# Kernel tuning notes

Hardware: AMD Instinct MI355X
Metric: run time of the kernel (lower is better)

## Reference

```python
import jax, jax.numpy as jnp
import numpy as np
import math

B, L, DIM, H = 2, 2048, 512, 8


def setup_inputs() -> dict:
    key = jax.random.key(0)
    ks = jax.random.split(key, 8)
    s = 0.02
    return {
        "x": jax.random.normal(ks[0], (B, L, DIM), dtype=jnp.float32),
        "Wq": jax.random.normal(ks[1], (DIM, DIM), dtype=jnp.float32) * s,
        "Wk": jax.random.normal(ks[2], (DIM, DIM), dtype=jnp.float32) * s,
        "Wv": jax.random.normal(ks[3], (DIM, DIM), dtype=jnp.float32) * s,
        "Wb": jax.random.normal(ks[4], (H, DIM), dtype=jnp.float32) * s,   # content_bias weight
        "mixing": jax.random.normal(ks[5], (H, DIM), dtype=jnp.float32) * 0.2,  # UNIFORM init, std=0.2
        "Wd": jax.random.normal(ks[6], (DIM, DIM), dtype=jnp.float32) * s,
        "bd": jax.random.normal(ks[7], (DIM,), dtype=jnp.float32) * s,
    }


def reference(x, Wq, Wk, Wv, Wb, mixing, Wd, bd):
    b, l, d = x.shape
    h = mixing.shape[0]
    dh = d // h
    q = x @ Wq.T                      # [B,L,D]
    k = x @ Wk.T                      # [B,S,D]
    v = (x @ Wv.T).reshape(b, l, h, dh).transpose(0, 2, 1, 3)  # [B,H,S,dh]
    # scores[b,h,l,s] = sum_d q[b,l,d] * mixing[h,d] * k[b,s,d]
    scores = jnp.einsum("bld,hd,bsd->bhls", q, mixing, k)
    # content bias: [B,S,H] -> broadcast over query positions as [B,H,1,S]
    cb = jnp.einsum("bsd,hd->bhs", x, Wb)
    scale = math.sqrt(d / h)  # attention_head_size = dim / num_heads
    scores = (scores + cb[:, :, None, :]) / scale
    probs = jax.nn.softmax(scores, axis=-1)   # dropout disabled (eval)
    ctx = jnp.einsum("bhls,bhsd->bhld", probs, v)  # [B,H,L,dh]
    ctx = ctx.transpose(0, 2, 1, 3).reshape(b, l, d)
    return ctx @ Wd.T + bd
```

## Files before the change

kernel.cpp:

```cpp
#include <hip/hip_runtime.h>

#define B_ 2
#define L_ 2048
#define D_ 512
#define H_ 8
#define S_ 2048

typedef __attribute__((ext_vector_type(8))) short short8;
typedef __attribute__((ext_vector_type(8))) unsigned short ushort8;
typedef __attribute__((ext_vector_type(4))) unsigned short ushort4v;
typedef __attribute__((ext_vector_type(4))) float f32x4;
typedef __attribute__((ext_vector_type(16))) float f32x16;
typedef __attribute__((ext_vector_type(4))) float float4v;
typedef __attribute__((ext_vector_type(8))) _Float16 half8;
typedef __attribute__((ext_vector_type(4))) _Float16 half4;

__device__ __forceinline__ unsigned short f2bf(float f) {
    unsigned u = __float_as_uint(f);
    u += 0x7FFF + ((u >> 16) & 1);
    return (unsigned short)(u >> 16);
}
__device__ __forceinline__ float bf2f(unsigned short s) {
    return __uint_as_float(((unsigned)s) << 16);
}
__device__ __forceinline__ unsigned char f2fp8(float f) {
    return (unsigned char)(__builtin_amdgcn_cvt_pk_fp8_f32(f, f, 0, false) & 0xff);
}
__device__ __forceinline__ long pack8fp8(const float* v) {
    int lo = __builtin_amdgcn_cvt_pk_fp8_f32(v[0], v[1], 0, false);
    lo = __builtin_amdgcn_cvt_pk_fp8_f32(v[2], v[3], lo, true);
    int hi = __builtin_amdgcn_cvt_pk_fp8_f32(v[4], v[5], 0, false);
    hi = __builtin_amdgcn_cvt_pk_fp8_f32(v[6], v[7], hi, true);
    union { int i[2]; long l; } u;
    u.i[0] = lo; u.i[1] = hi;
    return u.l;
}
__device__ __forceinline__ int swap23(int x) {
    return (x & ~12) | ((x & 4) << 1) | ((x & 8) >> 1);
}
__device__ __forceinline__ void async16(void* lds, const void* g) {
    __builtin_amdgcn_global_load_lds(
        (const __attribute__((address_space(1))) void*)(g),
        (__attribute__((address_space(3))) void*)(lds), 16, 0, 0);
}

__global__ __launch_bounds__(256) void cvt_cb(const float* __restrict__ x,
                                              const float* __restrict__ w0, const float* __restrict__ w1,
                                              const float* __restrict__ w2, const float* __restrict__ w3,
                                              const float* __restrict__ Wb,
                                              unsigned short* __restrict__ xb,
                                              unsigned short* __restrict__ d0, unsigned short* __restrict__ d1,
                                              unsigned short* __restrict__ d2, unsigned short* __restrict__ d3,
                                              float* __restrict__ cbf) {
    if (blockIdx.x < 3072) {
        int i = blockIdx.x * 256 + threadIdx.x;
        const float* s;
        unsigned short* d;
        int idx;
        if (i < 524288) { s = x; d = xb; idx = i; }
        else {
            int off = i - 524288;
            int wsel = off >> 16; idx = off & 65535;
            s = (wsel == 0) ? w0 : (wsel == 1) ? w1 : (wsel == 2) ? w2 : w3;
            d = (wsel == 0) ? d0 : (wsel == 1) ? d1 : (wsel == 2) ? d2 : d3;
        }
        float4v v = *(const float4v*)(s + (size_t)idx * 4);
        ushort4v o;
        o[0] = f2bf(v[0]); o[1] = f2bf(v[1]); o[2] = f2bf(v[2]); o[3] = f2bf(v[3]);
        *(ushort4v*)(d + (size_t)idx * 4) = o;
    } else {
        const int tid = threadIdx.x, w = tid >> 6, lane = tid & 63;
        const int row = (blockIdx.x - 3072) * 4 + w;
        const int h = lane >> 3, seg = lane & 7;
        const float* xp = x + (size_t)row * 512 + seg * 64;
        const float* wp = Wb + (size_t)h * 512 + seg * 64;
        float acc = 0.f;
        #pragma unroll
        for (int j = 0; j < 16; ++j) {
            float4v xv = *(const float4v*)(xp + j * 4);
            float4v wv = *(const float4v*)(wp + j * 4);
            acc += xv[0] * wv[0] + xv[1] * wv[1] + xv[2] * wv[2] + xv[3] * wv[3];
        }
        acc += __shfl_xor(acc, 1);
        acc += __shfl_xor(acc, 2);
        acc += __shfl_xor(acc, 4);
        if (seg == 0) {
            int b = row >> 11, s = row & 2047;
            int T = s >> 5, off = s & 31;
            int r2 = off & 3, k = off >> 2;
            int u = (k & 1) + ((k >> 2) << 1), hi2 = (k >> 1) & 1;
            int R = 4 * u + r2;
            cbf[((size_t)((b * 8 + h) * 64 + T)) * 32 + hi2 * 16 + R] = acc * 0.125f * 1.44269504f;
        }
    }
}

__device__ __forceinline__ void gemm128_core(const unsigned short* __restrict__ Ap,
                                             const unsigned short* __restrict__ Bp,
                                             short* sA, short* sB, int tid, f32x4 c[4][4]) {
    const int w = tid >> 6, lane = tid & 63, quad = lane >> 4, l15 = lane & 15;
    const int wm = (w >> 1) * 64, wn = (w & 1) * 64;
    for (int kc = 0; kc < 8; ++kc) {
        __syncthreads();
        #pragma unroll
        for (int j = 0; j < 4; ++j) {
            int i = tid + j * 256;
            int row = i >> 3, seg = i & 7;
            *(ushort8*)&sA[row * 72 + seg * 8] = *(const ushort8*)(Ap + (size_t)row * 512 + kc * 64 + seg * 8);
            *(ushort8*)&sB[row * 72 + seg * 8] = *(const ushort8*)(Bp + (size_t)row * 512 + kc * 64 + seg * 8);
        }
        __syncthreads();
        #pragma unroll
        for (int ks = 0; ks < 2; ++ks) {
            short8 a[4], b[4];
            #pragma unroll
            for (int ii = 0; ii < 4; ++ii)
                a[ii] = *(const short8*)&sA[(wm + ii * 16 + l15) * 72 + ks * 32 + quad * 8];
            #pragma unroll
            for (int jj = 0; jj < 4; ++jj)
                b[jj] = *(const short8*)&sB[(wn + jj * 16 + l15) * 72 + ks * 32 + quad * 8];
            #pragma unroll
            for (int ii = 0; ii < 4; ++ii)
                #pragma unroll
                for (int jj = 0; jj < 4; ++jj)
                    c[ii][jj] = __builtin_amdgcn_mfma_f32_16x16x32_bf16(a[ii], b[jj], c[ii][jj], 0, 0, 0);
        }
    }
}

__global__ __launch_bounds__(256) void gemm_qkv(const unsigned short* __restrict__ xb,
                                                const unsigned short* __restrict__ Wqb,
                                                const unsigned short* __restrict__ Wkb,
                                                const unsigned short* __restrict__ Wvb,
                                                unsigned short* __restrict__ qb,
                                                unsigned char* __restrict__ kpack8,
                                                unsigned short* __restrict__ vfrag) {
    __shared__ char sAB[2][32768];
    const int m0 = blockIdx.x * 128, n0 = blockIdx.y * 128, z = blockIdx.z;
    const unsigned short* Bsel = (z == 0) ? Wqb : ((z == 1) ? Wkb : Wvb);
    const int tid = threadIdx.x, w = tid >> 6, lane = tid & 63, quad = lane >> 4, l15 = lane & 15;
    const int wm = (w >> 1) * 64, wn = (w & 1) * 64;
    const char* Ab = (const char*)(xb + (size_t)m0 * 512);
    const char* Bb = (const char*)(Bsel + (size_t)n0 * 512);
    const int srow = tid >> 3;
    const int csw = (tid & 7) ^ (srow & 7);
    const size_t srcOff = (size_t)srow * 1024 + (size_t)csw * 16;
    auto stage = [&](int kc, int bi) {
        char* ba = &sAB[bi][0];
        #pragma unroll
        for (int j = 0; j < 4; ++j)
            async16(ba + j * 4096 + w * 1024, Ab + (size_t)j * 32768 + kc * 128 + srcOff);
        #pragma unroll
        for (int j = 0; j < 4; ++j)
            async16(ba + 16384 + j * 4096 + w * 1024, Bb + (size_t)j * 32768 + kc * 128 + srcOff);
    };

    f32x4 c[4][4];
    #pragma unroll
    for (int ii = 0; ii < 4; ++ii)
        #pragma unroll
        for (int jj = 0; jj < 4; ++jj) { f32x4 zv = {0.f, 0.f, 0.f, 0.f}; c[ii][jj] = zv; }

    stage(0, 0);
    for (int kc = 0; kc < 8; ++kc) {
        __syncthreads();
        if (kc < 7) stage(kc + 1, (kc + 1) & 1);
        const char* tA = &sAB[kc & 1][0];
        const char* tB = &sAB[kc & 1][16384];
        #pragma unroll
        for (int ks = 0; ks < 2; ++ks) {
            short8 a[4], b[4];
            #pragma unroll
            for (int ii = 0; ii < 4; ++ii) {
                int row = wm + ii * 16 + l15;
                a[ii] = *(const short8*)(tA + row * 128 + (((ks * 4 + quad) ^ (l15 & 7)) * 16));
            }
            #pragma unroll
            for (int jj = 0; jj < 4; ++jj) {
                int row = wn + jj * 16 + l15;
                b[jj] = *(const short8*)(tB + row * 128 + (((ks * 4 + quad) ^ (l15 & 7)) * 16));
            }
            #pragma unroll
            for (int ii = 0; ii < 4; ++ii)
                #pragma unroll
                for (int jj = 0; jj < 4; ++jj)
                    c[ii][jj] = __builtin_amdgcn_mfma_f32_16x16x32_bf16(a[ii], b[jj], c[ii][jj], 0, 0, 0);
        }
    }

    #pragma unroll
    for (int ii = 0; ii < 4; ++ii) {
        const int mb = m0 + wm + ii * 16 + quad * 4;
        const int bb = mb >> 11;
        if (z == 0) {
            #pragma unroll
            for (int jj = 0; jj < 4; ++jj) {
                int ncol = n0 + wn + jj * 16 + l15;
                #pragma unroll
                for (int r = 0; r < 4; ++r)
                    qb[(size_t)(mb + r) * 512 + ncol] = f2bf(c[ii][jj][r]);
            }
        } else if (z == 1) {
            #pragma unroll
            for (int jj = 0; jj < 4; ++jj) {
                int d = n0 + wn + jj * 16 + l15;
                int pair = d >> 5, fh = (d >> 4) & 1, hid = (d >> 3) & 1, jq = d & 7;
                #pragma unroll
                for (int r = 0; r < 4; ++r) {
                    int s = (mb + r) & 2047;
                    int t = s >> 5, rr = swap23(s & 31);
                    kpack8[(((size_t)(bb * 64 + t) * 16 + pair) << 10)
                           + (hid * 32 + rr) * 16 + fh * 8 + jq] = f2fp8(c[ii][jj][r] * 32.f);
                }
            }
        } else {
            const int hh = (n0 + wn) >> 6;
            const int s = mb & 2047;
            #pragma unroll
            for (int jj = 0; jj < 4; ++jj) {
                int dh = jj * 16 + l15;
                ushort4v o;
                o[0] = f2bf(c[ii][jj][0]); o[1] = f2bf(c[ii][jj][1]);
                o[2] = f2bf(c[ii][jj][2]); o[3] = f2bf(c[ii][jj][3]);
                size_t blk = ((size_t)(bb * H_ + hh) * 64 + (s >> 5)) * 4
                           + ((dh >> 5) * 2 + ((s >> 4) & 1));
                *(ushort4v*)(vfrag + blk * 512 + (dh & 31) * 8 + ((s >> 3) & 1) * 256 + (s & 7)) = o;
            }
        }
    }
}

__global__ __launch_bounds__(256) void gemm_out(const _Float16* __restrict__ Opart,
                                                const float* __restrict__ lpart,
                                                const unsigned short* __restrict__ Wdb,
                                                const float* __restrict__ bd,
                                                float* __restrict__ out) {
    __shared__ short sA[128 * 72];
    __shared__ short sB[128 * 72];
    const int m0 = blockIdx.x * 128, n0 = blockIdx.y * 128;
    const int tid = threadIdx.x, w = tid >> 6, lane = tid & 63, quad = lane >> 4, l15 = lane & 15;
    const int wm = (w >> 1) * 64, wn = (w & 1) * 64;
    f32x4 c[4][4];
    #pragma unroll
    for (int ii = 0; ii < 4; ++ii)
        #pragma unroll
        for (int jj = 0; jj < 4; ++jj) { f32x4 zv = {0.f, 0.f, 0.f, 0.f}; c[ii][jj] = zv; }
    for (int kc = 0; kc < 8; ++kc) {
        __syncthreads();
        #pragma unroll
        for (int j = 0; j < 4; ++j) {
            int i = tid + j * 256;
            int row = i >> 3, seg = i & 7;
            int gq = m0 + row;
            int b = gq >> 11, ql = gq & 2047, qq = ql & 127;
            int base = ((ql >> 7) << 5) | (kc << 2) | (b << 1);
            const _Float16* o0 = Opart + ((size_t)base << 13) + qq * 64 + seg * 8;
            float l = lpart[(size_t)base * 128 + qq] + lpart[(size_t)(base + 1) * 128 + qq];
            float inv = __builtin_amdgcn_rcpf(l);
            half8 v0 = *(const half8*)o0;
            half8 v1 = *(const half8*)(o0 + 8192);
            ushort8 ov;
            #pragma unroll
            for (int e = 0; e < 8; ++e)
                ov[e] = f2bf(((float)v0[e] + (float)v1[e]) * inv);
            *(ushort8*)&sA[row * 72 + seg * 8] = ov;
            *(ushort8*)&sB[row * 72 + seg * 8] =
                *(const ushort8*)(Wdb + (size_t)(n0 + row) * 512 + kc * 64 + seg * 8);
        }
        __syncthreads();
        #pragma unroll
        for (int ks = 0; ks < 2; ++ks) {
            short8 a[4], b2[4];
            #pragma unroll
            for (int ii = 0; ii < 4; ++ii)
                a[ii] = *(const short8*)&sA[(wm + ii * 16 + l15) * 72 + ks * 32 + quad * 8];
            #pragma unroll
            for (int jj = 0; jj < 4; ++jj)
                b2[jj] = *(const short8*)&sB[(wn + jj * 16 + l15) * 72 + ks * 32 + quad * 8];
            #pragma unroll
            for (int ii = 0; ii < 4; ++ii)
                #pragma unroll
                for (int jj = 0; jj < 4; ++jj)
                    c[ii][jj] = __builtin_amdgcn_mfma_f32_16x16x32_bf16(a[ii], b2[jj], c[ii][jj], 0, 0, 0);
        }
    }
    #pragma unroll
    for (int ii = 0; ii < 4; ++ii) {
        const int mb = m0 + wm + ii * 16 + quad * 4;
        #pragma unroll
        for (int jj = 0; jj < 4; ++jj) {
            int ncol = n0 + wn + jj * 16 + l15;
            float bias = bd[ncol];
            #pragma unroll
            for (int r = 0; r < 4; ++r)
                out[(size_t)(mb + r) * 512 + ncol] = c[ii][jj][r] + bias;
        }
    }
}

__global__ __launch_bounds__(256, 2) void flash_attn(const unsigned short* __restrict__ qb,
                                                     const unsigned char* __restrict__ kpack8,
                                                     const unsigned short* __restrict__ vfrag,
                                                     const float* __restrict__ cbf_all,
                                                     const float* __restrict__ mixing,
                                                     _Float16* __restrict__ Opart,
                                                     float* __restrict__ lpart) {
    __shared__ char sK[3][16384];
    const int bid = blockIdx.x;
    const int half = bid & 1, b = (bid >> 1) & 1, h = (bid >> 2) & 7, qt = bid >> 5;
    const int tid = threadIdx.x, w = tid >> 6, lane = tid & 63;
    const int l31 = lane & 31, hi = lane >> 5;
    const int q0 = qt * 128 + w * 32;
    const unsigned short* vfb = vfrag + ((size_t)(b * H_ + h) * 64 + half * 32) * 2048;
    const float* cbfb = cbf_all + ((size_t)((b * 8 + h) * 64 + half * 32)) * 32 + hi * 16;
    const float* mixh = mixing + h * D_;
    const float SC = 1.44269504f / 4096.0f;

    long qq[32];
    {
        const unsigned short* qrow = qb + ((size_t)(b * L_) + q0 + l31) * D_ + hi * 8;
        #pragma unroll
        for (int i = 0; i < 32; ++i) {
            ushort8 qv = *(const ushort8*)(qrow + i * 16);
            float4v ma = *(const float4v*)(mixh + i * 16 + hi * 8);
            float4v mb = *(const float4v*)(mixh + i * 16 + hi * 8 + 4);
            float v[8];
            v[0] = bf2f(qv[0]) * ma[0] * 16.f;
            v[1] = bf2f(qv[1]) * ma[1] * 16.f;
            v[2] = bf2f(qv[2]) * ma[2] * 16.f;
            v[3] = bf2f(qv[3]) * ma[3] * 16.f;
            v[4] = bf2f(qv[4]) * mb[0] * 16.f;
            v[5] = bf2f(qv[5]) * mb[1] * 16.f;
            v[6] = bf2f(qv[6]) * mb[2] * 16.f;
            v[7] = bf2f(qv[7]) * mb[3] * 16.f;
            qq[i] = pack8fp8(v);
        }
    }
    asm volatile("s_waitcnt vmcnt(0)" ::: "memory");

    f32x16 acco0, acco1;
    #pragma unroll
    for (int i = 0; i < 16; ++i) { acco0[i] = 0.f; acco1[i] = 0.f; }
    float lsum = 0.f;
    f32x16 aA0, aB0, aA1, aB1;
    short8 av00, av01, av10, av11;
    float4v cbf0, cbf1, cbf2, cbf3;

    auto stageK2 = [&](int t, int bi) {
        const char* src = (const char*)kpack8 + (((size_t)(b * 64 + half * 32 + t)) << 14);
        char* dst = &sK[bi][0];
        #pragma unroll
        for (int ii = 0; ii < 4; ++ii)
            async16(dst + w * 1024 + ii * 4096, src + w * 1024 + ii * 4096 + (size_t)lane * 16);
    };
    auto ldV = [&](int t) {
        const unsigned short* vp = vfb + (size_t)t * 2048 + lane * 8;
        av00 = *(const short8*)(vp);
        av01 = *(const short8*)(vp + 512);
        av10 = *(const short8*)(vp + 1024);
        av11 = *(const short8*)(vp + 1536);
        asm volatile("" ::: "memory");
    };
    auto ldCB = [&](int t) {
        const float* cp = cbfb + t * 32;
        cbf0 = *(const float4v*)(cp);
        cbf1 = *(const float4v*)(cp + 4);
        cbf2 = *(const float4v*)(cp + 8);
        cbf3 = *(const float4v*)(cp + 12);
        asm volatile("" ::: "memory");
    };
    auto cbfv = [&](int R) -> float {
        return (R < 4) ? cbf0[R & 3] : (R < 8) ? cbf1[R & 3] : (R < 12) ? cbf2[R & 3] : cbf3[R & 3];
    };
    auto pack_pv = [&](const float* pex) {
        union { unsigned int u[4]; short8 s8; } P0, P1;
        #pragma unroll
        for (int j = 0; j < 4; ++j) {
            P0.u[j] = __builtin_amdgcn_perm(__float_as_uint(pex[2 * j + 1]) + 0x8000u,
                                            __float_as_uint(pex[2 * j]) + 0x8000u, 0x07060302u);
            P1.u[j] = __builtin_amdgcn_perm(__float_as_uint(pex[8 + 2 * j + 1]) + 0x8000u,
                                            __float_as_uint(pex[8 + 2 * j]) + 0x8000u, 0x07060302u);
        }
        acco0 = __builtin_amdgcn_mfma_f32_32x32x16_bf16(av00, P0.s8, acco0, 0, 0, 0);
        acco0 = __builtin_amdgcn_mfma_f32_32x32x16_bf16(av01, P1.s8, acco0, 0, 0, 0);
        acco1 = __builtin_amdgcn_mfma_f32_32x32x16_bf16(av10, P0.s8, acco1, 0, 0, 0);
        acco1 = __builtin_amdgcn_mfma_f32_32x32x16_bf16(av11, P1.s8, acco1, 0, 0, 0);
    };
    auto tile_fused = [&](const char* buf, int T, f32x16& CA, f32x16& CB,
                          const f32x16& PA, const f32x16& PB) {
        __builtin_amdgcn_s_setprio(1);
        float pex[16];
        float lsA = 0.f, lsB = 0.f;
        #pragma unroll
        for (int fp = 0; fp < 16; ++fp) {
            const long* ap = (const long*)&buf[fp * 1024 + lane * 16];
            long a0 = ap[0], a1 = ap[1];
            CA = __builtin_amdgcn_mfma_f32_32x32x16_fp8_fp8(a0, qq[2 * fp], CA, 0, 0, 0);
            CB = __builtin_amdgcn_mfma_f32_32x32x16_fp8_fp8(a1, qq[2 * fp + 1], CB, 0, 0, 0);
            if (fp < 8) {
                float x0 = fmaf(PA[2 * fp] + PB[2 * fp], SC, cbfv(2 * fp));
                float x1 = fmaf(PA[2 * fp + 1] + PB[2 * fp + 1], SC, cbfv(2 * fp + 1));
                float e0, e1;
                asm("v_exp_f32 %0, %1" : "=v"(e0) : "v"(x0));
                asm("v_exp_f32 %0, %1" : "=v"(e1) : "v"(x1));
                pex[2 * fp] = e0; pex[2 * fp + 1] = e1;
                lsA += e0; lsB += e1;
            }
            if (fp == 8) { lsum += lsA + lsB; pack_pv(pex); }
            if (fp == 9)  ldV(T);
            if (fp == 10) ldCB(T);
        }
        __builtin_amdgcn_s_setprio(0);
    };
    auto tile_plain = [&](const char* buf, int T, f32x16& CA, f32x16& CB) {
        __builtin_amdgcn_s_setprio(1);
        #pragma unroll
        for (int fp = 0; fp < 16; ++fp) {
            const long* ap = (const long*)&buf[fp * 1024 + lane * 16];
            long a0 = ap[0], a1 = ap[1];
            CA = __builtin_amdgcn_mfma_f32_32x32x16_fp8_fp8(a0, qq[2 * fp], CA, 0, 0, 0);
            CB = __builtin_amdgcn_mfma_f32_32x32x16_fp8_fp8(a1, qq[2 * fp + 1], CB, 0, 0, 0);
            if (fp == 9)  ldV(T);
            if (fp == 10) ldCB(T);
        }
        __builtin_amdgcn_s_setprio(0);
    };
    auto sm_pv = [&](const f32x16& PA, const f32x16& PB) {
        float pex[16];
        float lsA = 0.f, lsB = 0.f;
        #pragma unroll
        for (int R = 0; R < 16; R += 2) {
            float x0 = fmaf(PA[R] + PB[R], SC, cbfv(R));
            float x1 = fmaf(PA[R + 1] + PB[R + 1], SC, cbfv(R + 1));
            float e0, e1;
            asm("v_exp_f32 %0, %1" : "=v"(e0) : "v"(x0));
            asm("v_exp_f32 %0, %1" : "=v"(e1) : "v"(x1));
            pex[R] = e0; pex[R + 1] = e1;
            lsA += e0; lsB += e1;
        }
        lsum += lsA + lsB;
        pack_pv(pex);
    };
    auto zero16 = [](f32x16& v) {
        #pragma unroll
        for (int i = 0; i < 16; ++i) v[i] = 0.f;
    };

    stageK2(0, 0); stageK2(1, 1);

    zero16(aA0); zero16(aB0);
    asm volatile("s_waitcnt vmcnt(4)" ::: "memory");
    __builtin_amdgcn_s_barrier();
    tile_plain(&sK[0][0], 0, aA0, aB0);
    stageK2(2, 2);

    int cur = 1;
    for (int t = 1; t <= 30; t += 2) {
        zero16(aA1); zero16(aB1);
        asm volatile("s_waitcnt vmcnt(4)" ::: "memory");
        __builtin_amdgcn_s_barrier();
        tile_fused(&sK[cur][0], t, aA1, aB1, aA0, aB0);
        if (t + 2 <= 31) stageK2(t + 2, (cur + 2 >= 3) ? cur - 1 : cur + 2);
        cur = (cur == 2) ? 0 : cur + 1;

        zero16(aA0); zero16(aB0);
        asm volatile("s_waitcnt vmcnt(4)" ::: "memory");
        __builtin_amdgcn_s_barrier();
        tile_fused(&sK[cur][0], t + 1, aA0, aB0, aA1, aB1);
        if (t + 3 <= 31) stageK2(t + 3, (cur + 2 >= 3) ? cur - 1 : cur + 2);
        cur = (cur == 2) ? 0 : cur + 1;
    }

    {
        zero16(aA1); zero16(aB1);
        asm volatile("s_waitcnt vmcnt(0)" ::: "memory");
        __builtin_amdgcn_s_barrier();
        tile_fused(&sK[cur][0], 31, aA1, aB1, aA0, aB0);
        asm volatile("s_waitcnt vmcnt(0)" ::: "memory");
        sm_pv(aA1, aB1);
    }

    lsum += __shfl_xor(lsum, 32);
    if (hi == 0) lpart[(size_t)bid * 128 + w * 32 + l31] = lsum;
    {
        _Float16* sO = (_Float16*)&sK[0][0];
        const int q = w * 32 + l31;
        #pragma unroll
        for (int u = 0; u < 4; ++u) {
            half4 v0, v1;
            v0[0] = (_Float16)acco0[4 * u];     v0[1] = (_Float16)acco0[4 * u + 1];
            v0[2] = (_Float16)acco0[4 * u + 2]; v0[3] = (_Float16)acco0[4 * u + 3];
            v1[0] = (_Float16)acco1[4 * u];     v1[1] = (_Float16)acco1[4 * u + 1];
            v1[2] = (_Float16)acco1[4 * u + 2]; v1[3] = (_Float16)acco1[4 * u + 3];
            *(half4*)&sO[q * 72 + u * 8 + 4 * hi]      = v0;
            *(half4*)&sO[q * 72 + 32 + u * 8 + 4 * hi] = v1;
        }
        const int qd = tid >> 1, hf = tid & 1;
        _Float16* dst = Opart + ((size_t)bid << 13) + qd * 64 + hf * 32;
        const _Float16* srcp = sO + qd * 72 + hf * 32;
        #pragma unroll
        for (int k = 0; k < 4; ++k)
            *(half8*)(dst + k * 8) = *(const half8*)(srcp + k * 8);
    }
}

extern "C" void kernel_launch(void* const* d_in, const int* in_sizes, int n_in,
                              void* d_out, int out_size, void* d_ws, size_t ws_size,
                              hipStream_t stream) {
    (void)in_sizes; (void)n_in; (void)out_size; (void)ws_size;
    const float* x      = (const float*)d_in[0];
    const float* Wq     = (const float*)d_in[1];
    const float* Wk     = (const float*)d_in[2];
    const float* Wv     = (const float*)d_in[3];
    const float* Wb     = (const float*)d_in[4];
    const float* mixing = (const float*)d_in[5];
    const float* Wd     = (const float*)d_in[6];
    const float* bd     = (const float*)d_in[7];
    float* out = (float*)d_out;

    char* ws = (char*)d_ws;
    const size_t MiB = 1048576;
    unsigned short* xb     = (unsigned short*)(ws);
    unsigned short* qb     = (unsigned short*)(ws + 4 * MiB);
    unsigned char*  kpack8 = (unsigned char*)(ws + 8 * MiB);
    unsigned short* vfrag  = (unsigned short*)(ws + 10 * MiB);
    unsigned short* Wqb    = (unsigned short*)(ws + 18 * MiB);
    unsigned short* Wkb    = (unsigned short*)(ws + 18 * MiB + 512 * 1024);
    unsigned short* Wvb    = (unsigned short*)(ws + 19 * MiB);
    unsigned short* Wdb    = (unsigned short*)(ws + 19 * MiB + 512 * 1024);
    float* cbuf            = (float*)(ws + 20 * MiB);
    float* lpart           = (float*)(ws + 20 * MiB + 256 * 1024);
    _Float16* Opart        = (_Float16*)(ws + 21 * MiB);

    cvt_cb<<<4096, 256, 0, stream>>>(x, Wq, Wk, Wv, Wd, Wb, xb, Wqb, Wkb, Wvb, Wdb, cbuf);
    gemm_qkv<<<dim3(32, 4, 3), 256, 0, stream>>>(xb, Wqb, Wkb, Wvb, qb, kpack8, vfrag);
    flash_attn<<<512, 256, 0, stream>>>(qb, kpack8, vfrag, cbuf, mixing, Opart, lpart);
    gemm_out<<<dim3(32, 4), 256, 0, stream>>>(Opart, lpart, Wdb, bd, out);
}
```

Before: 193.6 us.

## Split attention key range four ways across blocks and raise occupancy hint

Flash attention now splits the 2048 keys into four chunks of 512 instead of two of 1024 and launches 1024 blocks instead of 512. The output GEMM is updated to sum four partial outputs and four partial softmax denominators. Launch bounds rise to 3 blocks per CU, and the workspace is rearranged so the larger partial-output buffer overlaps the buffers that are dead by then. The aim is to fill the 256 CUs better and hide latency, at the cost of more partial-result traffic and more reduction work in gemm_out.

```diff
diff --git a/kernel.cpp b/kernel.cpp
--- a/kernel.cpp
+++ b/kernel.cpp
@@ -95,39 +95,6 @@
     }
 }
 
-__device__ __forceinline__ void gemm128_core(const unsigned short* __restrict__ Ap,
-                                             const unsigned short* __restrict__ Bp,
-                                             short* sA, short* sB, int tid, f32x4 c[4][4]) {
-    const int w = tid >> 6, lane = tid & 63, quad = lane >> 4, l15 = lane & 15;
-    const int wm = (w >> 1) * 64, wn = (w & 1) * 64;
-    for (int kc = 0; kc < 8; ++kc) {
-        __syncthreads();
-        #pragma unroll
-        for (int j = 0; j < 4; ++j) {
-            int i = tid + j * 256;
-            int row = i >> 3, seg = i & 7;
-            *(ushort8*)&sA[row * 72 + seg * 8] = *(const ushort8*)(Ap + (size_t)row * 512 + kc * 64 + seg * 8);
-            *(ushort8*)&sB[row * 72 + seg * 8] = *(const ushort8*)(Bp + (size_t)row * 512 + kc * 64 + seg * 8);
-        }
-        __syncthreads();
-        #pragma unroll
-        for (int ks = 0; ks < 2; ++ks) {
-            short8 a[4], b[4];
-            #pragma unroll
-            for (int ii = 0; ii < 4; ++ii)
-                a[ii] = *(const short8*)&sA[(wm + ii * 16 + l15) * 72 + ks * 32 + quad * 8];
-            #pragma unroll
-            for (int jj = 0; jj < 4; ++jj)
-                b[jj] = *(const short8*)&sB[(wn + jj * 16 + l15) * 72 + ks * 32 + quad * 8];
-            #pragma unroll
-            for (int ii = 0; ii < 4; ++ii)
-                #pragma unroll
-                for (int jj = 0; jj < 4; ++jj)
-                    c[ii][jj] = __builtin_amdgcn_mfma_f32_16x16x32_bf16(a[ii], b[jj], c[ii][jj], 0, 0, 0);
-        }
-    }
-}
-
 __global__ __launch_bounds__(256) void gemm_qkv(const unsigned short* __restrict__ xb,
                                                 const unsigned short* __restrict__ Wqb,
                                                 const unsigned short* __restrict__ Wkb,
@@ -188,6 +155,8 @@
         }
     }
 
+    const int tid2 = threadIdx.x;
+    (void)tid2;
     #pragma unroll
     for (int ii = 0; ii < 4; ++ii) {
         const int mb = m0 + wm + ii * 16 + quad * 4;
@@ -253,16 +222,19 @@
             int row = i >> 3, seg = i & 7;
             int gq = m0 + row;
             int b = gq >> 11, ql = gq & 2047, qq = ql & 127;
-            int base = ((ql >> 7) << 5) | (kc << 2) | (b << 1);
+            int base = ((ql >> 7) << 6) | (kc << 3) | (b << 2);
             const _Float16* o0 = Opart + ((size_t)base << 13) + qq * 64 + seg * 8;
-            float l = lpart[(size_t)base * 128 + qq] + lpart[(size_t)(base + 1) * 128 + qq];
+            float l = lpart[(size_t)base * 128 + qq] + lpart[(size_t)(base + 1) * 128 + qq]
+                    + lpart[(size_t)(base + 2) * 128 + qq] + lpart[(size_t)(base + 3) * 128 + qq];
             float inv = __builtin_amdgcn_rcpf(l);
             half8 v0 = *(const half8*)o0;
             half8 v1 = *(const half8*)(o0 + 8192);
+            half8 v2 = *(const half8*)(o0 + 16384);
+            half8 v3 = *(const half8*)(o0 + 24576);
             ushort8 ov;
             #pragma unroll
             for (int e = 0; e < 8; ++e)
-                ov[e] = f2bf(((float)v0[e] + (float)v1[e]) * inv);
+                ov[e] = f2bf(((float)v0[e] + (float)v1[e] + (float)v2[e] + (float)v3[e]) * inv);
             *(ushort8*)&sA[row * 72 + seg * 8] = ov;
             *(ushort8*)&sB[row * 72 + seg * 8] =
                 *(const ushort8*)(Wdb + (size_t)(n0 + row) * 512 + kc * 64 + seg * 8);
@@ -298,7 +270,7 @@
     }
 }
 
-__global__ __launch_bounds__(256, 2) void flash_attn(const unsigned short* __restrict__ qb,
+__global__ __launch_bounds__(256, 3) void flash_attn(const unsigned short* __restrict__ qb,
                                                      const unsigned char* __restrict__ kpack8,
                                                      const unsigned short* __restrict__ vfrag,
                                                      const float* __restrict__ cbf_all,
@@ -307,12 +279,12 @@
                                                      float* __restrict__ lpart) {
     __shared__ char sK[3][16384];
     const int bid = blockIdx.x;
-    const int half = bid & 1, b = (bid >> 1) & 1, h = (bid >> 2) & 7, qt = bid >> 5;
+    const int half = bid & 3, b = (bid >> 2) & 1, h = (bid >> 3) & 7, qt = bid >> 6;
     const int tid = threadIdx.x, w = tid >> 6, lane = tid & 63;
     const int l31 = lane & 31, hi = lane >> 5;
     const int q0 = qt * 128 + w * 32;
-    const unsigned short* vfb = vfrag + ((size_t)(b * H_ + h) * 64 + half * 32) * 2048;
-    const float* cbfb = cbf_all + ((size_t)((b * 8 + h) * 64 + half * 32)) * 32 + hi * 16;
+    const unsigned short* vfb = vfrag + ((size_t)(b * H_ + h) * 64 + half * 16) * 2048;
+    const float* cbfb = cbf_all + ((size_t)((b * 8 + h) * 64 + half * 16)) * 32 + hi * 16;
     const float* mixh = mixing + h * D_;
     const float SC = 1.44269504f / 4096.0f;
 
@@ -347,7 +319,7 @@
     float4v cbf0, cbf1, cbf2, cbf3;
 
     auto stageK2 = [&](int t, int bi) {
-        const char* src = (const char*)kpack8 + (((size_t)(b * 64 + half * 32 + t)) << 14);
+        const char* src = (const char*)kpack8 + (((size_t)(b * 64 + half * 16 + t)) << 14);
         char* dst = &sK[bi][0];
         #pragma unroll
         for (int ii = 0; ii < 4; ++ii)
@@ -455,19 +427,19 @@
     stageK2(2, 2);
 
     int cur = 1;
-    for (int t = 1; t <= 30; t += 2) {
+    for (int t = 1; t <= 14; t += 2) {
         zero16(aA1); zero16(aB1);
         asm volatile("s_waitcnt vmcnt(4)" ::: "memory");
         __builtin_amdgcn_s_barrier();
         tile_fused(&sK[cur][0], t, aA1, aB1, aA0, aB0);
-        if (t + 2 <= 31) stageK2(t + 2, (cur + 2 >= 3) ? cur - 1 : cur + 2);
+        if (t + 2 <= 15) stageK2(t + 2, (cur + 2 >= 3) ? cur - 1 : cur + 2);
         cur = (cur == 2) ? 0 : cur + 1;
 
         zero16(aA0); zero16(aB0);
         asm volatile("s_waitcnt vmcnt(4)" ::: "memory");
         __builtin_amdgcn_s_barrier();
         tile_fused(&sK[cur][0], t + 1, aA0, aB0, aA1, aB1);
-        if (t + 3 <= 31) stageK2(t + 3, (cur + 2 >= 3) ? cur - 1 : cur + 2);
+        if (t + 3 <= 15) stageK2(t + 3, (cur + 2 >= 3) ? cur - 1 : cur + 2);
         cur = (cur == 2) ? 0 : cur + 1;
     }
 
@@ -475,7 +447,7 @@
         zero16(aA1); zero16(aB1);
         asm volatile("s_waitcnt vmcnt(0)" ::: "memory");
         __builtin_amdgcn_s_barrier();
-        tile_fused(&sK[cur][0], 31, aA1, aB1, aA0, aB0);
+        tile_fused(&sK[cur][0], 15, aA1, aB1, aA0, aB0);
         asm volatile("s_waitcnt vmcnt(0)" ::: "memory");
         sm_pv(aA1, aB1);
     }
@@ -483,7 +455,7 @@
     lsum += __shfl_xor(lsum, 32);
     if (hi == 0) lpart[(size_t)bid * 128 + w * 32 + l31] = lsum;
     {
-        _Float16* sO = (_Float16*)&sK[0][0];
+        _Float16* sO = (_Float16*)&sK[1][0];
         const int q = w * 32 + l31;
         #pragma unroll
         for (int u = 0; u < 4; ++u) {
@@ -520,20 +492,21 @@
 
     char* ws = (char*)d_ws;
     const size_t MiB = 1048576;
+    const size_t KiB = 1024;
+    _Float16* Opart        = (_Float16*)(ws);
     unsigned short* xb     = (unsigned short*)(ws);
-    unsigned short* qb     = (unsigned short*)(ws + 4 * MiB);
-    unsigned char*  kpack8 = (unsigned char*)(ws + 8 * MiB);
-    unsigned short* vfrag  = (unsigned short*)(ws + 10 * MiB);
-    unsigned short* Wqb    = (unsigned short*)(ws + 18 * MiB);
-    unsigned short* Wkb    = (unsigned short*)(ws + 18 * MiB + 512 * 1024);
-    unsigned short* Wvb    = (unsigned short*)(ws + 19 * MiB);
-    unsigned short* Wdb    = (unsigned short*)(ws + 19 * MiB + 512 * 1024);
-    float* cbuf            = (float*)(ws + 20 * MiB);
-    float* lpart           = (float*)(ws + 20 * MiB + 256 * 1024);
-    _Float16* Opart        = (_Float16*)(ws + 21 * MiB);
+    unsigned short* Wqb    = (unsigned short*)(ws + 4 * MiB);
+    unsigned short* Wkb    = (unsigned short*)(ws + 4 * MiB + 512 * KiB);
+    unsigned short* Wvb    = (unsigned short*)(ws + 5 * MiB);
+    unsigned short* qb     = (unsigned short*)(ws + 16 * MiB);
+    unsigned char*  kpack8 = (unsigned char*)(ws + 20 * MiB);
+    unsigned short* vfrag  = (unsigned short*)(ws + 22 * MiB);
+    unsigned short* Wdb    = (unsigned short*)(ws + 26 * MiB);
+    float* cbuf            = (float*)(ws + 26 * MiB + 512 * KiB);
+    float* lpart           = (float*)(ws + 27 * MiB);
 
     cvt_cb<<<4096, 256, 0, stream>>>(x, Wq, Wk, Wv, Wd, Wb, xb, Wqb, Wkb, Wvb, Wdb, cbuf);
     gemm_qkv<<<dim3(32, 4, 3), 256, 0, stream>>>(xb, Wqb, Wkb, Wvb, qb, kpack8, vfrag);
-    flash_attn<<<512, 256, 0, stream>>>(qb, kpack8, vfrag, cbuf, mixing, Opart, lpart);
+    flash_attn<<<1024, 256, 0, stream>>>(qb, kpack8, vfrag, cbuf, mixing, Opart, lpart);
     gemm_out<<<dim3(32, 4), 256, 0, stream>>>(Opart, lpart, Wdb, bd, out);
 }
```

New measurement: 381.5 us. +97.1%, slower.

## Use MI355 scaled 32x32x64 fp8 MFMA for QK scores with repacked K layout

Applied to the files above, without the earlier changes.

Replaces the QK^T score computation, which used 32 fp8 32x32x16 MFMAs split across two accumulators, with 8 of the gfx950 scaled 32x32x64 f8f6f4 MFMAs using unit scales and a single accumulator. It also changes the fp8 K packing layout in the QKV GEMM epilogue and the Q fragment preparation so the operands match the new instruction. The goal is fewer MFMA issues, fewer LDS reads and fewer accumulator registers per tile. It also drops the dead gemm128_core helper. The risk is that the new layout indexing or operand ordering is wrong, and the longer single accumulation chain reduces instruction-level overlap.

```diff
diff --git a/kernel.cpp b/kernel.cpp
--- a/kernel.cpp
+++ b/kernel.cpp
@@ -14,6 +14,8 @@
 typedef __attribute__((ext_vector_type(4))) float float4v;
 typedef __attribute__((ext_vector_type(8))) _Float16 half8;
 typedef __attribute__((ext_vector_type(4))) _Float16 half4;
+typedef __attribute__((ext_vector_type(4))) int int4v;
+typedef __attribute__((ext_vector_type(8))) int int8v;
 
 __device__ __forceinline__ unsigned short f2bf(float f) {
     unsigned u = __float_as_uint(f);
@@ -95,39 +97,6 @@
     }
 }
 
-__device__ __forceinline__ void gemm128_core(const unsigned short* __restrict__ Ap,
-                                             const unsigned short* __restrict__ Bp,
-                                             short* sA, short* sB, int tid, f32x4 c[4][4]) {
-    const int w = tid >> 6, lane = tid & 63, quad = lane >> 4, l15 = lane & 15;
-    const int wm = (w >> 1) * 64, wn = (w & 1) * 64;
-    for (int kc = 0; kc < 8; ++kc) {
-        __syncthreads();
-        #pragma unroll
-        for (int j = 0; j < 4; ++j) {
-            int i = tid + j * 256;
-            int row = i >> 3, seg = i & 7;
-            *(ushort8*)&sA[row * 72 + seg * 8] = *(const ushort8*)(Ap + (size_t)row * 512 + kc * 64 + seg * 8);
-            *(ushort8*)&sB[row * 72 + seg * 8] = *(const ushort8*)(Bp + (size_t)row * 512 + kc * 64 + seg * 8);
-        }
-        __syncthreads();
-        #pragma unroll
-        for (int ks = 0; ks < 2; ++ks) {
-            short8 a[4], b[4];
-            #pragma unroll
-            for (int ii = 0; ii < 4; ++ii)
-                a[ii] = *(const short8*)&sA[(wm + ii * 16 + l15) * 72 + ks * 32 + quad * 8];
-            #pragma unroll
-            for (int jj = 0; jj < 4; ++jj)
-                b[jj] = *(const short8*)&sB[(wn + jj * 16 + l15) * 72 + ks * 32 + quad * 8];
-            #pragma unroll
-            for (int ii = 0; ii < 4; ++ii)
-                #pragma unroll
-                for (int jj = 0; jj < 4; ++jj)
-                    c[ii][jj] = __builtin_amdgcn_mfma_f32_16x16x32_bf16(a[ii], b[jj], c[ii][jj], 0, 0, 0);
-        }
-    }
-}
-
 __global__ __launch_bounds__(256) void gemm_qkv(const unsigned short* __restrict__ xb,
                                                 const unsigned short* __restrict__ Wqb,
                                                 const unsigned short* __restrict__ Wkb,
@@ -204,13 +173,13 @@
             #pragma unroll
             for (int jj = 0; jj < 4; ++jj) {
                 int d = n0 + wn + jj * 16 + l15;
-                int pair = d >> 5, fh = (d >> 4) & 1, hid = (d >> 3) & 1, jq = d & 7;
+                int f = d >> 6, ch = (d >> 4) & 1, kh = (d >> 5) & 1, j15 = d & 15;
                 #pragma unroll
                 for (int r = 0; r < 4; ++r) {
                     int s = (mb + r) & 2047;
                     int t = s >> 5, rr = swap23(s & 31);
-                    kpack8[(((size_t)(bb * 64 + t) * 16 + pair) << 10)
-                           + (hid * 32 + rr) * 16 + fh * 8 + jq] = f2fp8(c[ii][jj][r] * 32.f);
+                    kpack8[((size_t)(bb * 64 + t) << 14)
+                           + f * 2048 + ch * 1024 + (kh * 32 + rr) * 16 + j15] = f2fp8(c[ii][jj][r] * 32.f);
                 }
             }
         } else {
@@ -316,24 +285,30 @@
     const float* mixh = mixing + h * D_;
     const float SC = 1.44269504f / 4096.0f;
 
-    long qq[32];
+    int8v qf8v[8];
     {
-        const unsigned short* qrow = qb + ((size_t)(b * L_) + q0 + l31) * D_ + hi * 8;
-        #pragma unroll
-        for (int i = 0; i < 32; ++i) {
-            ushort8 qv = *(const ushort8*)(qrow + i * 16);
-            float4v ma = *(const float4v*)(mixh + i * 16 + hi * 8);
-            float4v mb = *(const float4v*)(mixh + i * 16 + hi * 8 + 4);
-            float v[8];
-            v[0] = bf2f(qv[0]) * ma[0] * 16.f;
-            v[1] = bf2f(qv[1]) * ma[1] * 16.f;
-            v[2] = bf2f(qv[2]) * ma[2] * 16.f;
-            v[3] = bf2f(qv[3]) * ma[3] * 16.f;
-            v[4] = bf2f(qv[4]) * mb[0] * 16.f;
-            v[5] = bf2f(qv[5]) * mb[1] * 16.f;
-            v[6] = bf2f(qv[6]) * mb[2] * 16.f;
-            v[7] = bf2f(qv[7]) * mb[3] * 16.f;
-            qq[i] = pack8fp8(v);
+        const unsigned short* qrow = qb + ((size_t)(b * L_) + q0 + l31) * D_;
+        #pragma unroll
+        for (int f = 0; f < 8; ++f) {
+            union { long l[4]; int8v v; } qu;
+            #pragma unroll
+            for (int g = 0; g < 4; ++g) {
+                int d0 = f * 64 + hi * 32 + g * 8;
+                ushort8 qv = *(const ushort8*)(qrow + d0);
+                float4v ma = *(const float4v*)(mixh + d0);
+                float4v mb2 = *(const float4v*)(mixh + d0 + 4);
+                float v[8];
+                v[0] = bf2f(qv[0]) * ma[0] * 16.f;
+                v[1] = bf2f(qv[1]) * ma[1] * 16.f;
+                v[2] = bf2f(qv[2]) * ma[2] * 16.f;
+                v[3] = bf2f(qv[3]) * ma[3] * 16.f;
+                v[4] = bf2f(qv[4]) * mb2[0] * 16.f;
+                v[5] = bf2f(qv[5]) * mb2[1] * 16.f;
+                v[6] = bf2f(qv[6]) * mb2[2] * 16.f;
+                v[7] = bf2f(qv[7]) * mb2[3] * 16.f;
+                qu.l[g] = pack8fp8(v);
+            }
+            qf8v[f] = qu.v;
         }
     }
     asm volatile("s_waitcnt vmcnt(0)" ::: "memory");
@@ -342,7 +317,7 @@
     #pragma unroll
     for (int i = 0; i < 16; ++i) { acco0[i] = 0.f; acco1[i] = 0.f; }
     float lsum = 0.f;
-    f32x16 aA0, aB0, aA1, aB1;
+    f32x16 aS0, aS1;
     short8 av00, av01, av10, av11;
     float4v cbf0, cbf1, cbf2, cbf3;
 
@@ -386,52 +361,61 @@
         acco1 = __builtin_amdgcn_mfma_f32_32x32x16_bf16(av10, P0.s8, acco1, 0, 0, 0);
         acco1 = __builtin_amdgcn_mfma_f32_32x32x16_bf16(av11, P1.s8, acco1, 0, 0, 0);
     };
-    auto tile_fused = [&](const char* buf, int T, f32x16& CA, f32x16& CB,
-                          const f32x16& PA, const f32x16& PB) {
+    auto ldA = [&](const char* buf, int f) -> int8v {
+        int4v lo = *(const int4v*)&buf[f * 2048 + lane * 16];
+        int4v ah = *(const int4v*)&buf[f * 2048 + 1024 + lane * 16];
+        int8v a;
+        a[0] = lo[0]; a[1] = lo[1]; a[2] = lo[2]; a[3] = lo[3];
+        a[4] = ah[0]; a[5] = ah[1]; a[6] = ah[2]; a[7] = ah[3];
+        return a;
+    };
+    auto tile_fused = [&](const char* buf, int T, f32x16& C, const f32x16& P) {
         __builtin_amdgcn_s_setprio(1);
         float pex[16];
         float lsA = 0.f, lsB = 0.f;
         #pragma unroll
-        for (int fp = 0; fp < 16; ++fp) {
-            const long* ap = (const long*)&buf[fp * 1024 + lane * 16];
-            long a0 = ap[0], a1 = ap[1];
-            CA = __builtin_amdgcn_mfma_f32_32x32x16_fp8_fp8(a0, qq[2 * fp], CA, 0, 0, 0);
-            CB = __builtin_amdgcn_mfma_f32_32x32x16_fp8_fp8(a1, qq[2 * fp + 1], CB, 0, 0, 0);
-            if (fp < 8) {
-                float x0 = fmaf(PA[2 * fp] + PB[2 * fp], SC, cbfv(2 * fp));
-                float x1 = fmaf(PA[2 * fp + 1] + PB[2 * fp + 1], SC, cbfv(2 * fp + 1));
-                float e0, e1;
-                asm("v_exp_f32 %0, %1" : "=v"(e0) : "v"(x0));
-                asm("v_exp_f32 %0, %1" : "=v"(e1) : "v"(x1));
-                pex[2 * fp] = e0; pex[2 * fp + 1] = e1;
-                lsA += e0; lsB += e1;
-            }
-            if (fp == 8) { lsum += lsA + lsB; pack_pv(pex); }
-            if (fp == 9)  ldV(T);
-            if (fp == 10) ldCB(T);
+        for (int f = 0; f < 8; ++f) {
+            int8v a = ldA(buf, f);
+            C = __builtin_amdgcn_mfma_scale_f32_32x32x64_f8f6f4(
+                    a, qf8v[f], C, 0, 0, 0, 0x7F7F7F7F, 0, 0x7F7F7F7F);
+            if (f < 4) {
+                #pragma unroll
+                for (int j = 0; j < 4; j += 2) {
+                    int R = 4 * f + j;
+                    float x0 = fmaf(P[R], SC, cbfv(R));
+                    float x1 = fmaf(P[R + 1], SC, cbfv(R + 1));
+                    float e0, e1;
+                    asm("v_exp_f32 %0, %1" : "=v"(e0) : "v"(x0));
+                    asm("v_exp_f32 %0, %1" : "=v"(e1) : "v"(x1));
+                    pex[R] = e0; pex[R + 1] = e1;
+                    lsA += e0; lsB += e1;
+                }
+            }
+            if (f == 4) { lsum += lsA + lsB; pack_pv(pex); }
+            if (f == 5)  ldV(T);
+            if (f == 6)  ldCB(T);
         }
         __builtin_amdgcn_s_setprio(0);
     };
-    auto tile_plain = [&](const char* buf, int T, f32x16& CA, f32x16& CB) {
+    auto tile_plain = [&](const char* buf, int T, f32x16& C) {
         __builtin_amdgcn_s_setprio(1);
         #pragma unroll
-        for (int fp = 0; fp < 16; ++fp) {
-            const long* ap = (const long*)&buf[fp * 1024 + lane * 16];
-            long a0 = ap[0], a1 = ap[1];
-            CA = __builtin_amdgcn_mfma_f32_32x32x16_fp8_fp8(a0, qq[2 * fp], CA, 0, 0, 0);
-            CB = __builtin_amdgcn_mfma_f32_32x32x16_fp8_fp8(a1, qq[2 * fp + 1], CB, 0, 0, 0);
-            if (fp == 9)  ldV(T);
-            if (fp == 10) ldCB(T);
+        for (int f = 0; f < 8; ++f) {
+            int8v a = ldA(buf, f);
+            C = __builtin_amdgcn_mfma_scale_f32_32x32x64_f8f6f4(
+                    a, qf8v[f], C, 0, 0, 0, 0x7F7F7F7F, 0, 0x7F7F7F7F);
+            if (f == 5) ldV(T);
+            if (f == 6) ldCB(T);
         }
         __builtin_amdgcn_s_setprio(0);
     };
-    auto sm_pv = [&](const f32x16& PA, const f32x16& PB) {
+    auto sm_pv = [&](const f32x16& P) {
         float pex[16];
         float lsA = 0.f, lsB = 0.f;
         #pragma unroll
         for (int R = 0; R < 16; R += 2) {
-            float x0 = fmaf(PA[R] + PB[R], SC, cbfv(R));
-            float x1 = fmaf(PA[R + 1] + PB[R + 1], SC, cbfv(R + 1));
+            float x0 = fmaf(P[R], SC, cbfv(R));
+            float x1 = fmaf(P[R + 1], SC, cbfv(R + 1));
             float e0, e1;
             asm("v_exp_f32 %0, %1" : "=v"(e0) : "v"(x0));
             asm("v_exp_f32 %0, %1" : "=v"(e1) : "v"(x1));
@@ -448,36 +432,36 @@
 
     stageK2(0, 0); stageK2(1, 1);
 
-    zero16(aA0); zero16(aB0);
+    zero16(aS0);
     asm volatile("s_waitcnt vmcnt(4)" ::: "memory");
     __builtin_amdgcn_s_barrier();
-    tile_plain(&sK[0][0], 0, aA0, aB0);
+    tile_plain(&sK[0][0], 0, aS0);
     stageK2(2, 2);
 
     int cur = 1;
     for (int t = 1; t <= 30; t += 2) {
-        zero16(aA1); zero16(aB1);
+        zero16(aS1);
         asm volatile("s_waitcnt vmcnt(4)" ::: "memory");
         __builtin_amdgcn_s_barrier();
-        tile_fused(&sK[cur][0], t, aA1, aB1, aA0, aB0);
+        tile_fused(&sK[cur][0], t, aS1, aS0);
         if (t + 2 <= 31) stageK2(t + 2, (cur + 2 >= 3) ? cur - 1 : cur + 2);
         cur = (cur == 2) ? 0 : cur + 1;
 
-        zero16(aA0); zero16(aB0);
+        zero16(aS0);
         asm volatile("s_waitcnt vmcnt(4)" ::: "memory");
         __builtin_amdgcn_s_barrier();
-        tile_fused(&sK[cur][0], t + 1, aA0, aB0, aA1, aB1);
+        tile_fused(&sK[cur][0], t + 1, aS0, aS1);
         if (t + 3 <= 31) stageK2(t + 3, (cur + 2 >= 3) ? cur - 1 : cur + 2);
         cur = (cur == 2) ? 0 : cur + 1;
     }
 
     {
-        zero16(aA1); zero16(aB1);
+        zero16(aS1);
         asm volatile("s_waitcnt vmcnt(0)" ::: "memory");
         __builtin_amdgcn_s_barrier();
-        tile_fused(&sK[cur][0], 31, aA1, aB1, aA0, aB0);
+        tile_fused(&sK[cur][0], 31, aS1, aS0);
         asm volatile("s_waitcnt vmcnt(0)" ::: "memory");
-        sm_pv(aA1, aB1);
+        sm_pv(aS1);
     }
 
     lsum += __shfl_xor(lsum, 32);
```

Measured after the change: 182.7 us. 5.6% less time.
